# Optimization experiments

Measured on AMD Instinct MI355X. Metric: run time of the kernel, lower is better.

Reference implementation:

```python
import jax, jax.numpy as jnp
import numpy as np

RD = 3  # rec_depth


def _conv_block(x, w, b):
    # x: [B, T, C] -> Conv1d(same padding for odd kernel) + ReLU.
    # AdaptiveMaxPool1d(T) on a length-T input is the identity, so it is omitted.
    pad = (w.shape[-1] - 1) // 2
    xc = jnp.transpose(x, (0, 2, 1))  # [B, C, T]
    out = jax.lax.conv_general_dilated(xc, w, (1,), [(pad, pad)],
                                       dimension_numbers=('NCH', 'OIH', 'NCH'))
    out = jax.nn.relu(out + b[None, :, None])
    return jnp.transpose(out, (0, 2, 1))  # [B, T, n_filters]


def _rhn_cell(x_in, s, WH, WT, RHw, RHb, RTw, RTb):
    # Coupled-gate RHN cell: RD micro-steps of gated highway updates.
    preds = []
    for l in range(RD):
        if l == 0:
            h = jnp.tanh(x_in @ WH + s @ RHw[l] + RHb[l])
            t = jax.nn.sigmoid(x_in @ WT + s @ RTw[l] + RTb[l])
        else:
            h = jnp.tanh(s @ RHw[l] + RHb[l])
            t = jax.nn.sigmoid(s @ RTw[l] + RTb[l])
        s = h * t + (1.0 - t) * s
        preds.append(s)
    return s, preds


def _forward(x, y, conv0_w, conv0_b, conv1_w, conv1_b, c2e_w, c2e_b,
             enc_WH, enc_WT, enc_RHw, enc_RHb, enc_RTw, enc_RTb,
             dec_WH, dec_WT, dec_RHw, dec_RHb, dec_RTw, dec_RTb,
             Tk_w, Uk_w, Uk_b, vk_w, vk_b,
             Wt_w, Vt_w, Vt_b, W_w, W_b, V_w, V_b):
    x = _conv_block(x, conv0_w, conv0_b)
    x = _conv_block(x, conv1_w, conv1_b)
    x = x @ c2e_w + c2e_b                          # [B, T, enc_input_size]
    B, T, _ = x.shape
    NE = enc_WH.shape[1]
    ND = dec_WH.shape[1]

    # ---- RHN encoder: scan over time, emit state after every rec-depth step ----
    def enc_step(s, x_t):
        s, preds = _rhn_cell(x_t, s, enc_WH, enc_WT, enc_RHw, enc_RHb, enc_RTw, enc_RTb)
        return s, jnp.stack(preds, axis=-1)        # [B, NE, RD]

    _, hw = jax.lax.scan(enc_step, jnp.zeros((B, NE), x.dtype), jnp.transpose(x, (1, 0, 2)))
    h = jnp.transpose(hw, (1, 0, 2, 3))            # [B, T, NE, RD] == h_T_L

    # Encoder-side attention projections are decoder-time-invariant: precompute.
    Uh = jnp.einsum('btnr,rnm->rbtm', h, Uk_w) + Uk_b[:, None, None, :]  # [RD, B, T, NE]

    # ---- attentive RHN decoder ----
    def dec_step(carry, y_t):
        s, _ = carry
        Ts = jnp.einsum('bd,rdm->rbm', s, Tk_w)    # T_k(s) broadcast over T
        e = jnp.einsum('rbtm,rm->rbt', jnp.tanh(Uh + Ts[:, :, None, :]), vk_w) \
            + vk_b[:, None, None]                  # [RD, B, T]
        alpha = jax.nn.softmax(e, axis=-1)         # softmax over T
        d = jnp.einsum('rbt,btnr->rbn', alpha, h)  # [RD, B, NE]
        d = jnp.transpose(d, (1, 0, 2)).reshape(B, -1)  # [B, RD*NE], k-major blocks
        y_til = y_t @ Wt_w + d @ Vt_w + Vt_b
        s, _ = _rhn_cell(y_til, s, dec_WH, dec_WT, dec_RHw, dec_RHb, dec_RTw, dec_RTb)
        return (s, d), None

    init = (jnp.zeros((B, ND), x.dtype), jnp.zeros((B, RD * NE), x.dtype))
    (s, d), _ = jax.lax.scan(dec_step, init, jnp.transpose(y, (1, 0, 2)))
    return s @ W_w + W_b + d @ V_w + V_b           # [B, target_feats]


def setup_inputs() -> dict:
    ks = jax.random.split(jax.random.key(0), 24)
    B, T, F, TF = 256, 256, 16, 1
    NF, EI, NE, ND, FS = 64, 64, 128, 128, 5

    def rn(i, shape, s=0.1):
        return jax.random.normal(ks[i], shape, jnp.float32) * s

    z = lambda *shape: jnp.zeros(shape, jnp.float32)
    return {
        'x': jax.random.normal(ks[0], (B, T, F), jnp.float32),
        'y': jax.random.normal(ks[1], (B, T, TF), jnp.float32),
        'conv0_w': rn(2, (NF, F, FS)), 'conv0_b': z(NF),
        'conv1_w': rn(3, (NF, NF, FS)), 'conv1_b': z(NF),
        'c2e_w': rn(4, (NF, EI)), 'c2e_b': z(EI),
        'enc_WH': rn(5, (EI, NE)), 'enc_WT': rn(6, (EI, NE)),
        'enc_RHw': rn(7, (RD, NE, NE)), 'enc_RHb': z(RD, NE),
        'enc_RTw': rn(8, (RD, NE, NE)), 'enc_RTb': z(RD, NE),
        'dec_WH': rn(9, (TF, ND)), 'dec_WT': rn(10, (TF, ND)),
        'dec_RHw': rn(11, (RD, ND, ND)), 'dec_RHb': z(RD, ND),
        'dec_RTw': rn(12, (RD, ND, ND)), 'dec_RTb': z(RD, ND),
        'Tk_w': rn(13, (RD, ND, NE)),
        'Uk_w': rn(14, (RD, NE, NE)), 'Uk_b': z(RD, NE),
        'vk_w': rn(15, (RD, NE)), 'vk_b': z(RD),
        'Wt_w': rn(16, (TF, TF)),
        'Vt_w': rn(17, (RD * NE, TF)), 'Vt_b': z(TF),
        'W_w': rn(18, (ND, TF)), 'W_b': z(TF),
        'V_w': rn(19, (RD * NE, TF)), 'V_b': z(TF),
    }


def reference(x, y, conv0_w, conv0_b, conv1_w, conv1_b, c2e_w, c2e_b,
              enc_WH, enc_WT, enc_RHw, enc_RHb, enc_RTw, enc_RTb,
              dec_WH, dec_WT, dec_RHw, dec_RHb, dec_RTw, dec_RTb,
              Tk_w, Uk_w, Uk_b, vk_w, vk_b,
              Wt_w, Vt_w, Vt_b, W_w, W_b, V_w, V_b):
    return _forward(x, y, conv0_w, conv0_b, conv1_w, conv1_b, c2e_w, c2e_b,
                    enc_WH, enc_WT, enc_RHw, enc_RHb, enc_RTw, enc_RTb,
                    dec_WH, dec_WT, dec_RHw, dec_RHb, dec_RTw, dec_RTb,
                    Tk_w, Uk_w, Uk_b, vk_w, vk_b,
                    Wt_w, Vt_w, Vt_b, W_w, W_b, V_w, V_b)
```

## Files before the change

kernel.cpp:

```cpp
#include <hip/hip_runtime.h>
#include <cstdint>

#define DEV __device__ __forceinline__

typedef unsigned short ushort8 __attribute__((ext_vector_type(8)));
typedef unsigned int uint32;

#if __has_builtin(__builtin_amdgcn_rcpf)
DEV float rcp_fast(float x) { return __builtin_amdgcn_rcpf(x); }
#else
DEV float rcp_fast(float x) { return 1.f / x; }
#endif
#if __has_builtin(__builtin_amdgcn_exp2f)
DEV float exp2_fast(float x) { return __builtin_amdgcn_exp2f(x); }
#else
DEV float exp2_fast(float x) { return exp2f(x); }
#endif

#define SCALE2LOG2E 2.8853900817779268f
#define LOG2E 1.4426950408889634f

DEV float tanh_fast(float x) {
  float z = exp2_fast(x * SCALE2LOG2E);
  return 1.f - 2.f * rcp_fast(z + 1.f);
}
DEV float sigmoid_fast(float x) {
  return rcp_fast(1.f + exp2_fast(-LOG2E * x));
}

DEV unsigned short f2bf(float f) {
  uint32 u = __float_as_uint(f);
  u += 0x7FFFu + ((u >> 16) & 1u);
  return (unsigned short)(u >> 16);
}
DEV float bf2f(unsigned short s) { return __uint_as_float(((uint32)s) << 16); }
DEV float bf2f_lo(uint32 u) { return __uint_as_float(u << 16); }
DEV float bf2f_hi(uint32 u) { return __uint_as_float(u & 0xFFFF0000u); }

__global__ __launch_bounds__(256) void k_prep(const float* __restrict__ RHw,
                                              const float* __restrict__ RTw,
                                              uint32* __restrict__ out) {
  int i = blockIdx.x * 256 + threadIdx.x;
  if (i >= 49152) return;
  int g = i / 24576, rem = i % 24576;
  int l = rem / 8192, n2 = (rem >> 7) & 63, m = rem & 127;
  const float* W = g ? RTw : RHw;
  float w0 = W[(size_t)(l * 128 + 2 * n2) * 128 + m];
  float w1 = W[(size_t)(l * 128 + 2 * n2 + 1) * 128 + m];
  out[i] = (uint32)f2bf(w0) | ((uint32)f2bf(w1) << 16);
}

__global__ __launch_bounds__(256) void k_conv0(
    const float* __restrict__ x, const float* __restrict__ w,
    const float* __restrict__ bias, float* __restrict__ out) {
  __shared__ float wl[16 * 5 * 64];
  __shared__ float xl[68 * 16];
  const int blk = blockIdx.x;
  const int b = blk >> 2, tt = blk & 3;
  const int tid = threadIdx.x;
  for (int i = tid; i < 5120; i += 256) {
    int o = i / 80, rem = i % 80, ii = rem / 5, kk = rem % 5;
    wl[(ii * 5 + kk) * 64 + o] = w[i];
  }
  const int t0 = tt * 64;
  for (int i = tid; i < 68 * 16; i += 256) {
    int row = i >> 4, c = i & 15;
    int t = t0 - 2 + row;
    xl[i] = (t >= 0 && t < 256) ? x[((b << 8) + t) * 16 + c] : 0.f;
  }
  __syncthreads();
  const int o = tid & 63, tr = tid >> 6;
  for (int j = 0; j < 16; ++j) {
    int tl = tr * 16 + j;
    float acc = bias[o];
#pragma unroll
    for (int kk = 0; kk < 5; ++kk)
#pragma unroll
      for (int ii = 0; ii < 16; ++ii)
        acc += xl[(tl + kk) * 16 + ii] * wl[(ii * 5 + kk) * 64 + o];
    out[((b << 8) + t0 + tl) * 64 + o] = fmaxf(acc, 0.f);
  }
}

__global__ __launch_bounds__(256) void k_conv1(
    const float* __restrict__ in0, const float* __restrict__ w,
    const float* __restrict__ bias, float* __restrict__ out) {
  __shared__ float wl[64 * 5 * 64];
  __shared__ float xl[68 * 64];
  const int blk = blockIdx.x;
  const int b = blk >> 2, tt = blk & 3;
  const int tid = threadIdx.x;
  for (int i = tid; i < 64 * 5 * 64; i += 256) {
    int o = i / 320, rem = i % 320, ii = rem / 5, kk = rem % 5;
    wl[(ii * 5 + kk) * 64 + o] = w[i];
  }
  const int t0 = tt * 64;
  for (int i = tid; i < 68 * 64; i += 256) {
    int row = i >> 6, c = i & 63;
    int t = t0 - 2 + row;
    xl[i] = (t >= 0 && t < 256) ? in0[((b << 8) + t) * 64 + c] : 0.f;
  }
  __syncthreads();
  const int o = tid & 63, tr = tid >> 6;
  for (int j = 0; j < 16; ++j) {
    int tl = tr * 16 + j;
    float acc = bias[o];
    for (int kk = 0; kk < 5; ++kk) {
#pragma unroll 16
      for (int ii = 0; ii < 64; ++ii)
        acc += xl[(tl + kk) * 64 + ii] * wl[(ii * 5 + kk) * 64 + o];
    }
    out[((b << 8) + t0 + tl) * 64 + o] = fmaxf(acc, 0.f);
  }
}

__global__ __launch_bounds__(256) void k_c2e_proj(
    const float* __restrict__ in1, const float* __restrict__ cw,
    const float* __restrict__ cb, const float* __restrict__ WH,
    const float* __restrict__ WT, float* __restrict__ xph,
    float* __restrict__ xpt) {
  __shared__ float xin[64 * 64];
  __shared__ float w1[64 * 64];
  __shared__ float xe[64 * 64];
  __shared__ float wh[64 * 128];
  __shared__ float wt[64 * 128];
  const int blk = blockIdx.x;
  const int b = blk >> 2, tt = blk & 3;
  const int tid = threadIdx.x;
  for (int i = tid; i < 4096; i += 256) {
    xin[i] = in1[(size_t)(((b << 8) + tt * 64)) * 64 + i];
    w1[i] = cw[i];
  }
  for (int i = tid; i < 8192; i += 256) {
    wh[i] = WH[i];
    wt[i] = WT[i];
  }
  __syncthreads();
  {
    const int o = tid & 63, tr = tid >> 6;
    for (int j = 0; j < 16; ++j) {
      int tl = tr * 16 + j;
      float acc = cb[o];
#pragma unroll 16
      for (int k = 0; k < 64; ++k) acc += xin[tl * 64 + k] * w1[k * 64 + o];
      xe[tl * 64 + o] = acc;
    }
  }
  __syncthreads();
  {
    const int m = tid & 127, hf = tid >> 7;
    for (int j = 0; j < 32; ++j) {
      int tl = hf * 32 + j;
      float a0 = 0.f, a1 = 0.f;
#pragma unroll 16
      for (int k = 0; k < 64; ++k) {
        float xv = xe[tl * 64 + k];
        a0 += xv * wh[k * 128 + m];
        a1 += xv * wt[k * 128 + m];
      }
      size_t oidx = (size_t)((b << 8) + tt * 64 + tl) * 128 + m;
      xph[oidx] = a0;
      xpt[oidx] = a1;
    }
  }
}

__global__ __launch_bounds__(512, 2) void k_encoder(
    const float* __restrict__ xph, const float* __restrict__ xpt,
    const float* __restrict__ RHw, const float* __restrict__ RHb,
    const float* __restrict__ RTw, const float* __restrict__ RTb,
    unsigned short* __restrict__ h_bf) {
  const int b = blockIdx.x;
  const int tid = threadIdx.x;
  const int g = tid >> 8;
  const int m = (tid >> 1) & 127;
  const int hf = tid & 1;
  const float* W = g ? RTw : RHw;
  const float* Bb = g ? RTb : RHb;
  const float* XP = g ? xpt : xph;
  float wreg[3][64];
#pragma unroll
  for (int l = 0; l < 3; ++l)
#pragma unroll
    for (int j = 0; j < 64; ++j)
      wreg[l][j] = W[(size_t)(l * 128 + hf * 64 + j) * 128 + m];
  float bias[3];
#pragma unroll
  for (int l = 0; l < 3; ++l) bias[l] = Bb[l * 128 + m];

  __shared__ float s_lds[128];
  __shared__ float hg[128];
  __shared__ float tg[128];
  if (tid < 128) s_lds[tid] = 0.f;
  __syncthreads();

  for (int t = 0; t < 256; ++t) {
    const float xp = XP[(size_t)((b << 8) + t) * 128 + m];
#pragma unroll
    for (int l = 0; l < 3; ++l) {
      float acc = (hf == 0) ? (bias[l] + (l == 0 ? xp : 0.f)) : 0.f;
      const float* sp = s_lds + hf * 64;
#pragma unroll
      for (int j = 0; j < 64; ++j) acc += sp[j] * wreg[l][j];
      float tot = acc + __shfl_xor(acc, 1);
      if (hf == 0) {
        if (g == 0) hg[m] = tanh_fast(tot);
        else        tg[m] = sigmoid_fast(tot);
      }
      __syncthreads();
      if (tid < 128) {
        float tv = tg[tid];
        float sn = hg[tid] * tv + (1.f - tv) * s_lds[tid];
        s_lds[tid] = sn;
        h_bf[((size_t)(b * 3 + l) * 256 + t) * 128 + tid] = f2bf(sn);
      }
      __syncthreads();
    }
  }
}

__global__ __launch_bounds__(256, 2) void k_uh(
    const unsigned short* __restrict__ h_bf, const float* __restrict__ Uk_w,
    const float* __restrict__ Uk_b, unsigned short* __restrict__ Uh_bf) {
  __shared__ float wl[128 * 128];
  __shared__ float hl[32 * 128];
  const int blk = blockIdx.x;
  const int b = blk / 3, r = blk % 3;
  const int tid = threadIdx.x;
  for (int i = tid; i < 16384; i += 256) wl[i] = Uk_w[(size_t)r * 16384 + i];
  const int m = tid & 127, tr = tid >> 7;
  const float ub = Uk_b[r * 128 + m];
  for (int tt = 0; tt < 8; ++tt) {
    const size_t hbase = ((size_t)(b * 3 + r) * 256 + tt * 32) * 128;
    __syncthreads();
    const ushort8* hv = (const ushort8*)(h_bf + hbase);
    for (int i = tid; i < 512; i += 256) {
      ushort8 u = hv[i];
#pragma unroll
      for (int j = 0; j < 8; ++j) hl[i * 8 + j] = bf2f(u[j]);
    }
    __syncthreads();
    for (int j = 0; j < 16; ++j) {
      int tl = tr * 16 + j;
      float acc = ub;
#pragma unroll 16
      for (int n = 0; n < 128; ++n) acc += hl[tl * 128 + n] * wl[n * 128 + m];
      Uh_bf[hbase + (size_t)tl * 128 + m] = f2bf(acc * SCALE2LOG2E);
    }
  }
}

__global__ __launch_bounds__(768) void k_hv(
    const unsigned short* __restrict__ h_bf, const float* __restrict__ Vt_w,
    const float* __restrict__ V_w, float* __restrict__ hv,
    float* __restrict__ hv2) {
  __shared__ float vt[384], vw[384];
  const int b = blockIdx.x, tid = threadIdx.x;
  if (tid < 384) {
    vt[tid] = Vt_w[tid];
    vw[tid] = V_w[tid];
  }
  __syncthreads();
  const int r = tid >> 8;
  const uint2* hp = (const uint2*)(h_bf + ((size_t)b * 768 + tid) * 128);
  const float* vtp = vt + r * 128;
  const float* vwp = vw + r * 128;
  float a1 = 0.f, a2 = 0.f;
#pragma unroll 8
  for (int q = 0; q < 32; ++q) {
    uint2 u = hp[q];
    int m = q * 4;
    float h0 = bf2f_lo(u.x), h1 = bf2f_hi(u.x);
    float h2 = bf2f_lo(u.y), h3 = bf2f_hi(u.y);
    a1 += vtp[m] * h0 + vtp[m + 1] * h1 + vtp[m + 2] * h2 + vtp[m + 3] * h3;
    a2 += vwp[m] * h0 + vwp[m + 1] * h1 + vwp[m + 2] * h2 + vwp[m + 3] * h3;
  }
  hv[(size_t)b * 768 + tid] = a1;
  hv2[(size_t)b * 768 + tid] = a2;
}

__global__ __launch_bounds__(1024, 4) void k_decoder(
    const float* __restrict__ y, const unsigned short* __restrict__ Uh_bf,
    const float* __restrict__ hv_g, const float* __restrict__ hv2_g,
    const float* __restrict__ Tk_w, const float* __restrict__ vk_w,
    const float* __restrict__ vk_b, const float* __restrict__ Wt_w,
    const float* __restrict__ Vt_b, const float* __restrict__ WHd,
    const float* __restrict__ WTd, const uint32* __restrict__ cellw,
    const float* __restrict__ RHb, const float* __restrict__ RTb,
    const float* __restrict__ W_w, const float* __restrict__ W_b,
    const float* __restrict__ V_b, float* __restrict__ out) {
  const int b = blockIdx.x, tid = threadIdx.x;

  __shared__ uint32 tk_lds[24576];
  __shared__ __align__(8) float Ts_lds[3 * 136];
  __shared__ __align__(8) float vk_pad[3 * 136];
  __shared__ __align__(8) float a_lds[768];
  __shared__ float hv_lds[768], hv2_lds[768];
  __shared__ __align__(8) float s_lds[128];
  __shared__ float cpart[8 * 128];
  __shared__ float bias_lds[1024];
  __shared__ float y_lds[256];
  __shared__ float redN[12], redD[12], redN2[12];
  __shared__ float svk_lds[3];
  __shared__ float ytil_lds;

  for (int i = tid; i < 24576; i += 1024) {
    int r = i >> 13, rem = i & 8191, j = rem >> 7, m = rem & 127;
    float g0 = Tk_w[(size_t)r * 16384 + (2 * j) * 128 + m] * SCALE2LOG2E;
    float g1 = Tk_w[(size_t)r * 16384 + (2 * j + 1) * 128 + m] * SCALE2LOG2E;
    tk_lds[r * 8192 + m * 64 + (j ^ (m & 31))] =
        (uint32)f2bf(g0) | ((uint32)f2bf(g1) << 16);
  }
  if (tid < 384) {
    int r = tid >> 7, m = tid & 127;
    vk_pad[r * 136 + (m >> 5) * 34 + (m & 31)] = -2.f * vk_w[tid];
    bias_lds[tid] = RHb[tid];
    bias_lds[384 + tid] = RTb[tid];
  }
  if (tid < 3) {
    float sv = vk_b[tid];
    for (int m = 0; m < 128; ++m) sv += vk_w[tid * 128 + m];
    svk_lds[tid] = sv;
  }
  if (tid < 128) {
    bias_lds[768 + tid] = WHd[tid];
    bias_lds[896 + tid] = WTd[tid];
    s_lds[tid] = 0.f;
  }
  if (tid < 256) y_lds[tid] = y[(b << 8) + tid];
  if (tid < 768) {
    hv_lds[tid] = hv_g[(size_t)b * 768 + tid];
    hv2_lds[tid] = hv2_g[(size_t)b * 768 + tid];
  }
  const float wt0 = Wt_w[0], vtb0 = Vt_b[0];

  const int t_e4 = tid >> 2, q4 = tid & 3;
  uint32 ureg[3][16];
#pragma unroll
  for (int r = 0; r < 3; ++r) {
    const uint4* up = (const uint4*)(Uh_bf +
        ((size_t)(b * 3 + r) * 256 + t_e4) * 128 + q4 * 32);
#pragma unroll
    for (int q = 0; q < 4; ++q) {
      uint4 v = up[q];
      ureg[r][4 * q + 0] = v.x;
      ureg[r][4 * q + 1] = v.y;
      ureg[r][4 * q + 2] = v.z;
      ureg[r][4 * q + 3] = v.w;
    }
  }
  uint32 zr;
  asm volatile("s_mov_b32 %0, 0" : "=s"(zr));
#pragma unroll
  for (int r = 0; r < 3; ++r)
#pragma unroll
    for (int q = 0; q < 16; ++q) ureg[r][q] ^= zr;
  __syncthreads();

  const int lane = tid & 63, wv = tid >> 6;
  const int r3t = (tid >> 8) & 3, m2 = (tid >> 1) & 127, p2 = tid & 1;
  const int gc = tid >> 9, ch = (tid >> 7) & 3, mc = tid & 127;
  const uint32* Wc = cellw + gc * 24576 + mc;
  const int n2base = ch * 16;

  for (int step = 0; step < 256; ++step) {
    if (tid < 768) {
      const uint32* tkp = tk_lds + r3t * 8192 + m2 * 64;
      const int swz = m2 & 31;
      const float* sp = s_lds + p2 * 64;
      const int jb = p2 * 32;
      float acc = 0.f;
#pragma unroll 8
      for (int jj = 0; jj < 32; ++jj) {
        uint32 w = tkp[(jb + jj) ^ swz];
        float2 sv = *(const float2*)(sp + 2 * jj);
        acc += sv.x * bf2f_lo(w) + sv.y * bf2f_hi(w);
      }
      float tot = acc + __shfl_xor(acc, 1);
      if (p2 == 0) Ts_lds[r3t * 136 + (m2 >> 5) * 34 + (m2 & 31)] = tot;
    }
    __syncthreads();
    {
      float er[3];
#pragma unroll
      for (int r = 0; r < 3; ++r) {
        const float2* ts2 = (const float2*)(Ts_lds + r * 136 + q4 * 34);
        const float2* vk2 = (const float2*)(vk_pad + r * 136 + q4 * 34);
        float acc0 = 0.f, acc1 = 0.f;
#pragma unroll
        for (int j = 0; j < 16; ++j) {
          uint32 w = ureg[r][j];
          float2 t2 = ts2[j], v2 = vk2[j];
          float z0 = exp2_fast(bf2f_lo(w) + t2.x);
          float z1 = exp2_fast(bf2f_hi(w) + t2.y);
          acc0 += v2.x * rcp_fast(z0 + 1.f);
          acc1 += v2.y * rcp_fast(z1 + 1.f);
        }
        float a = acc0 + acc1;
        a += __shfl_xor(a, 1);
        a += __shfl_xor(a, 2);
        er[r] = a;
      }
      if (q4 == 0) {
#pragma unroll
        for (int r = 0; r < 3; ++r) a_lds[r * 256 + t_e4] = er[r] + svk_lds[r];
      }
    }
    __syncthreads();
    {
      float pn = 0.f, pd = 0.f, pn2 = 0.f;
      if (tid < 768) {
        float p = __expf(a_lds[tid]);
        pd = p;
        pn = p * hv_lds[tid];
        if (step == 255) pn2 = p * hv2_lds[tid];
      }
#pragma unroll
      for (int off = 32; off; off >>= 1) {
        pn += __shfl_xor(pn, off);
        pd += __shfl_xor(pd, off);
      }
      if (step == 255) {
#pragma unroll
        for (int off = 32; off; off >>= 1) pn2 += __shfl_xor(pn2, off);
        if (lane == 0 && wv < 12) redN2[wv] = pn2;
      }
      if (lane == 0 && wv < 12) {
        redN[wv] = pn;
        redD[wv] = pd;
      }
    }
    __syncthreads();
    const float2* sp2 = (const float2*)s_lds;
#pragma unroll
    for (int l = 0; l < 3; ++l) {
      {
        float acc = 0.f;
        const uint32* wp = Wc + (size_t)(l * 64 + n2base) * 128;
#pragma unroll 8
        for (int n2 = 0; n2 < 16; ++n2) {
          uint32 w = wp[(size_t)n2 * 128];
          float2 sv = sp2[n2base + n2];
          acc += sv.x * bf2f_lo(w) + sv.y * bf2f_hi(w);
        }
        cpart[(gc * 4 + ch) * 128 + mc] = acc;
        if (l == 0 && tid == 0) {
          float yt = y_lds[step] * wt0 + vtb0;
#pragma unroll
          for (int r = 0; r < 3; ++r) {
            float ns = redN[4 * r] + redN[4 * r + 1] + redN[4 * r + 2] + redN[4 * r + 3];
            float ds = redD[4 * r] + redD[4 * r + 1] + redD[4 * r + 2] + redD[4 * r + 3];
            yt += ns * rcp_fast(ds);
          }
          ytil_lds = yt;
        }
      }
      __syncthreads();
      if (tid < 128) {
        float ha = cpart[tid] + cpart[128 + tid] + cpart[256 + tid] +
                   cpart[384 + tid] + bias_lds[l * 128 + tid];
        float ta = cpart[512 + tid] + cpart[640 + tid] + cpart[768 + tid] +
                   cpart[896 + tid] + bias_lds[384 + l * 128 + tid];
        if (l == 0) {
          float yt = ytil_lds;
          ha += yt * bias_lds[768 + tid];
          ta += yt * bias_lds[896 + tid];
        }
        float hvv = tanh_fast(ha);
        float tv = sigmoid_fast(ta);
        s_lds[tid] = hvv * tv + (1.f - tv) * s_lds[tid];
      }
      __syncthreads();
    }
  }
  if (tid < 64) {
    float acc = s_lds[tid] * W_w[tid] + s_lds[tid + 64] * W_w[tid + 64];
#pragma unroll
    for (int off = 32; off; off >>= 1) acc += __shfl_xor(acc, off);
    if (tid == 0) {
      float o = acc + W_b[0] + V_b[0];
#pragma unroll
      for (int r = 0; r < 3; ++r) {
        float ns = redN2[4 * r] + redN2[4 * r + 1] + redN2[4 * r + 2] + redN2[4 * r + 3];
        float ds = redD[4 * r] + redD[4 * r + 1] + redD[4 * r + 2] + redD[4 * r + 3];
        o += ns * rcp_fast(ds);
      }
      out[b] = o;
    }
  }
}

extern "C" void kernel_launch(void* const* d_in, const int* in_sizes, int n_in,
                              void* d_out, int out_size, void* d_ws,
                              size_t ws_size, hipStream_t stream) {
  (void)in_sizes; (void)n_in; (void)out_size; (void)ws_size;
  const float* x    = (const float*)d_in[0];
  const float* y    = (const float*)d_in[1];
  const float* c0w  = (const float*)d_in[2];
  const float* c0b  = (const float*)d_in[3];
  const float* c1w  = (const float*)d_in[4];
  const float* c1b  = (const float*)d_in[5];
  const float* c2ew = (const float*)d_in[6];
  const float* c2eb = (const float*)d_in[7];
  const float* eWH  = (const float*)d_in[8];
  const float* eWT  = (const float*)d_in[9];
  const float* eRHw = (const float*)d_in[10];
  const float* eRHb = (const float*)d_in[11];
  const float* eRTw = (const float*)d_in[12];
  const float* eRTb = (const float*)d_in[13];
  const float* dWH  = (const float*)d_in[14];
  const float* dWT  = (const float*)d_in[15];
  const float* dRHw = (const float*)d_in[16];
  const float* dRHb = (const float*)d_in[17];
  const float* dRTw = (const float*)d_in[18];
  const float* dRTb = (const float*)d_in[19];
  const float* Tk   = (const float*)d_in[20];
  const float* Ukw  = (const float*)d_in[21];
  const float* Ukb  = (const float*)d_in[22];
  const float* vkw  = (const float*)d_in[23];
  const float* vkb  = (const float*)d_in[24];
  const float* Wtw  = (const float*)d_in[25];
  const float* Vtw  = (const float*)d_in[26];
  const float* Vtb  = (const float*)d_in[27];
  const float* Ww   = (const float*)d_in[28];
  const float* Wb   = (const float*)d_in[29];
  const float* Vw   = (const float*)d_in[30];
  const float* Vb   = (const float*)d_in[31];
  float* out = (float*)d_out;
  float* ws = (float*)d_ws;

  unsigned short* h_bf  = (unsigned short*)ws;
  unsigned short* Uh_bf = (unsigned short*)(ws + 12582912);
  float* xph = ws + 12582912;
  float* xpt = ws + 20971520;
  float* c0o = ws + 29360128;
  float* hv  = ws + 29360128;
  float* hv2 = ws + 30146560;
  float* c1o = ws + 33554432;
  uint32* cellw = (uint32*)(ws + 37748736);

  k_prep<<<192, 256, 0, stream>>>(dRHw, dRTw, cellw);
  k_conv0<<<1024, 256, 0, stream>>>(x, c0w, c0b, c0o);
  k_conv1<<<1024, 256, 0, stream>>>(c0o, c1w, c1b, c1o);
  k_c2e_proj<<<1024, 256, 0, stream>>>(c1o, c2ew, c2eb, eWH, eWT, xph, xpt);
  k_encoder<<<256, 512, 0, stream>>>(xph, xpt, eRHw, eRHb, eRTw, eRTb, h_bf);
  k_uh<<<768, 256, 0, stream>>>(h_bf, Ukw, Ukb, Uh_bf);
  k_hv<<<256, 768, 0, stream>>>(h_bf, Vtw, Vw, hv, hv2);
  k_decoder<<<256, 1024, 0, stream>>>(y, Uh_bf, hv, hv2, Tk, vkw, vkb, Wtw,
                                      Vtb, dWH, dWT, cellw, dRHb, dRTb,
                                      Ww, Wb, Vb, out);
}
```

Before: 4.901 ms.

## Restructure decoder cell matvec with shuffle reductions and double-buffered state

The decoder RHN cell matvec now gives each group of 8 threads one output row, with each thread reading contiguous uint4 weight vectors under a new k_prep layout. Partial sums are combined with warp shuffles instead of an LDS partial buffer plus a second phase. This removes one __syncthreads per micro-step, and a double-buffered state vector makes that safe. Ts and vk are interleaved into float4 entries so the attention-score loop issues fewer, wider LDS loads. Every thread also computes ytil redundantly instead of one thread writing it to shared memory.

```diff
diff --git a/kernel.cpp b/kernel.cpp
--- a/kernel.cpp
+++ b/kernel.cpp
@@ -43,7 +43,8 @@
   int i = blockIdx.x * 256 + threadIdx.x;
   if (i >= 49152) return;
   int g = i / 24576, rem = i % 24576;
-  int l = rem / 8192, n2 = (rem >> 7) & 63, m = rem & 127;
+  int l = rem / 8192, rem2 = rem & 8191;
+  int m = rem2 >> 6, n2 = rem2 & 63;
   const float* W = g ? RTw : RHw;
   float w0 = W[(size_t)(l * 128 + 2 * n2) * 128 + m];
   float w1 = W[(size_t)(l * 128 + 2 * n2 + 1) * 128 + m];
@@ -292,17 +293,14 @@
   const int b = blockIdx.x, tid = threadIdx.x;
 
   __shared__ uint32 tk_lds[24576];
-  __shared__ __align__(8) float Ts_lds[3 * 136];
-  __shared__ __align__(8) float vk_pad[3 * 136];
+  __shared__ __align__(16) float4 tsvk4[3 * 4 * 17];
+  __shared__ __align__(16) float s_buf[2][128];
   __shared__ __align__(8) float a_lds[768];
   __shared__ float hv_lds[768], hv2_lds[768];
-  __shared__ __align__(8) float s_lds[128];
-  __shared__ float cpart[8 * 128];
   __shared__ float bias_lds[1024];
   __shared__ float y_lds[256];
   __shared__ float redN[12], redD[12], redN2[12];
   __shared__ float svk_lds[3];
-  __shared__ float ytil_lds;
 
   for (int i = tid; i < 24576; i += 1024) {
     int r = i >> 13, rem = i & 8191, j = rem >> 7, m = rem & 127;
@@ -311,21 +309,26 @@
     tk_lds[r * 8192 + m * 64 + (j ^ (m & 31))] =
         (uint32)f2bf(g0) | ((uint32)f2bf(g1) << 16);
   }
-  if (tid < 384) {
-    int r = tid >> 7, m = tid & 127;
-    vk_pad[r * 136 + (m >> 5) * 34 + (m & 31)] = -2.f * vk_w[tid];
-    bias_lds[tid] = RHb[tid];
-    bias_lds[384 + tid] = RTb[tid];
+  if (tid < 192) {
+    int r = tid >> 6, rem = tid & 63, q4i = rem >> 4, j = rem & 15;
+    int mb = q4i * 32 + 2 * j;
+    tsvk4[(r * 4 + q4i) * 17 + j].z = -2.f * vk_w[r * 128 + mb];
+    tsvk4[(r * 4 + q4i) * 17 + j].w = -2.f * vk_w[r * 128 + mb + 1];
   }
   if (tid < 3) {
     float sv = vk_b[tid];
     for (int m = 0; m < 128; ++m) sv += vk_w[tid * 128 + m];
     svk_lds[tid] = sv;
   }
+  if (tid < 384) {
+    bias_lds[tid] = RHb[tid];
+    bias_lds[384 + tid] = RTb[tid];
+  }
   if (tid < 128) {
     bias_lds[768 + tid] = WHd[tid];
     bias_lds[896 + tid] = WTd[tid];
-    s_lds[tid] = 0.f;
+    s_buf[0][tid] = 0.f;
+    s_buf[1][tid] = 0.f;
   }
   if (tid < 256) y_lds[tid] = y[(b << 8) + tid];
   if (tid < 768) {
@@ -359,42 +362,45 @@
 
   const int lane = tid & 63, wv = tid >> 6;
   const int r3t = (tid >> 8) & 3, m2 = (tid >> 1) & 127, p2 = tid & 1;
-  const int gc = tid >> 9, ch = (tid >> 7) & 3, mc = tid & 127;
-  const uint32* Wc = cellw + gc * 24576 + mc;
-  const int n2base = ch * 16;
+  const int mC = tid >> 3, sub = tid & 7, gC = sub >> 2, chC = sub & 3;
+  const uint32* wb0 = cellw + ((size_t)(gC * 3) << 13) + (mC << 6) + (chC << 4);
+  float* scur = s_buf[0];
+  float* snxt = s_buf[1];
 
   for (int step = 0; step < 256; ++step) {
     if (tid < 768) {
       const uint32* tkp = tk_lds + r3t * 8192 + m2 * 64;
       const int swz = m2 & 31;
-      const float* sp = s_lds + p2 * 64;
+      const float4* sp4 = (const float4*)scur + p2 * 16;
       const int jb = p2 * 32;
       float acc = 0.f;
 #pragma unroll 8
-      for (int jj = 0; jj < 32; ++jj) {
-        uint32 w = tkp[(jb + jj) ^ swz];
-        float2 sv = *(const float2*)(sp + 2 * jj);
-        acc += sv.x * bf2f_lo(w) + sv.y * bf2f_hi(w);
+      for (int k = 0; k < 16; ++k) {
+        float4 f4 = sp4[k];
+        uint32 w0 = tkp[(jb + 2 * k) ^ swz];
+        uint32 w1 = tkp[(jb + 2 * k + 1) ^ swz];
+        acc += f4.x * bf2f_lo(w0) + f4.y * bf2f_hi(w0) +
+               f4.z * bf2f_lo(w1) + f4.w * bf2f_hi(w1);
       }
       float tot = acc + __shfl_xor(acc, 1);
-      if (p2 == 0) Ts_lds[r3t * 136 + (m2 >> 5) * 34 + (m2 & 31)] = tot;
+      if (p2 == 0)
+        ((float*)&tsvk4[(r3t * 4 + (m2 >> 5)) * 17 + ((m2 >> 1) & 15)])[m2 & 1] = tot;
     }
     __syncthreads();
     {
       float er[3];
 #pragma unroll
       for (int r = 0; r < 3; ++r) {
-        const float2* ts2 = (const float2*)(Ts_lds + r * 136 + q4 * 34);
-        const float2* vk2 = (const float2*)(vk_pad + r * 136 + q4 * 34);
+        const float4* tv4 = tsvk4 + (r * 4 + q4) * 17;
         float acc0 = 0.f, acc1 = 0.f;
 #pragma unroll
         for (int j = 0; j < 16; ++j) {
           uint32 w = ureg[r][j];
-          float2 t2 = ts2[j], v2 = vk2[j];
-          float z0 = exp2_fast(bf2f_lo(w) + t2.x);
-          float z1 = exp2_fast(bf2f_hi(w) + t2.y);
-          acc0 += v2.x * rcp_fast(z0 + 1.f);
-          acc1 += v2.y * rcp_fast(z1 + 1.f);
+          float4 q = tv4[j];
+          float z0 = exp2_fast(bf2f_lo(w) + q.x);
+          float z1 = exp2_fast(bf2f_hi(w) + q.y);
+          acc0 += q.z * rcp_fast(z0 + 1.f);
+          acc1 += q.w * rcp_fast(z1 + 1.f);
         }
         float a = acc0 + acc1;
         a += __shfl_xor(a, 1);
@@ -431,50 +437,48 @@
       }
     }
     __syncthreads();
-    const float2* sp2 = (const float2*)s_lds;
+    float ytil = y_lds[step] * wt0 + vtb0;
+#pragma unroll
+    for (int r = 0; r < 3; ++r) {
+      float ns = redN[4 * r] + redN[4 * r + 1] + redN[4 * r + 2] + redN[4 * r + 3];
+      float ds = redD[4 * r] + redD[4 * r + 1] + redD[4 * r + 2] + redD[4 * r + 3];
+      ytil += ns * rcp_fast(ds);
+    }
 #pragma unroll
     for (int l = 0; l < 3; ++l) {
-      {
-        float acc = 0.f;
-        const uint32* wp = Wc + (size_t)(l * 64 + n2base) * 128;
-#pragma unroll 8
-        for (int n2 = 0; n2 < 16; ++n2) {
-          uint32 w = wp[(size_t)n2 * 128];
-          float2 sv = sp2[n2base + n2];
-          acc += sv.x * bf2f_lo(w) + sv.y * bf2f_hi(w);
-        }
-        cpart[(gc * 4 + ch) * 128 + mc] = acc;
-        if (l == 0 && tid == 0) {
-          float yt = y_lds[step] * wt0 + vtb0;
-#pragma unroll
-          for (int r = 0; r < 3; ++r) {
-            float ns = redN[4 * r] + redN[4 * r + 1] + redN[4 * r + 2] + redN[4 * r + 3];
-            float ds = redD[4 * r] + redD[4 * r + 1] + redD[4 * r + 2] + redD[4 * r + 3];
-            yt += ns * rcp_fast(ds);
-          }
-          ytil_lds = yt;
-        }
-      }
+      const uint4* wp = (const uint4*)(wb0 + (l << 13));
+      const float4* sp4 = (const float4*)scur + chC * 8;
+      float acc = 0.f;
+#pragma unroll
+      for (int q = 0; q < 4; ++q) {
+        uint4 w4 = wp[q];
+        float4 fa = sp4[2 * q], fb = sp4[2 * q + 1];
+        acc += fa.x * bf2f_lo(w4.x) + fa.y * bf2f_hi(w4.x) +
+               fa.z * bf2f_lo(w4.y) + fa.w * bf2f_hi(w4.y) +
+               fb.x * bf2f_lo(w4.z) + fb.y * bf2f_hi(w4.z) +
+               fb.z * bf2f_lo(w4.w) + fb.w * bf2f_hi(w4.w);
+      }
+      acc += __shfl_xor(acc, 1);
+      acc += __shfl_xor(acc, 2);
+      float other = __shfl_xor(acc, 4);
+      float hsum = gC ? other : acc;
+      float tsum = gC ? acc : other;
+      float s_old = scur[mC];
+      float ha = hsum + bias_lds[l * 128 + mC];
+      float ta = tsum + bias_lds[384 + l * 128 + mC];
+      if (l == 0) {
+        ha += ytil * bias_lds[768 + mC];
+        ta += ytil * bias_lds[896 + mC];
+      }
+      float hvv = tanh_fast(ha);
+      float tv = sigmoid_fast(ta);
+      if (sub == 0) snxt[mC] = hvv * tv + (1.f - tv) * s_old;
       __syncthreads();
-      if (tid < 128) {
-        float ha = cpart[tid] + cpart[128 + tid] + cpart[256 + tid] +
-                   cpart[384 + tid] + bias_lds[l * 128 + tid];
-        float ta = cpart[512 + tid] + cpart[640 + tid] + cpart[768 + tid] +
-                   cpart[896 + tid] + bias_lds[384 + l * 128 + tid];
-        if (l == 0) {
-          float yt = ytil_lds;
-          ha += yt * bias_lds[768 + tid];
-          ta += yt * bias_lds[896 + tid];
-        }
-        float hvv = tanh_fast(ha);
-        float tv = sigmoid_fast(ta);
-        s_lds[tid] = hvv * tv + (1.f - tv) * s_lds[tid];
-      }
-      __syncthreads();
+      float* tmp = scur; scur = snxt; snxt = tmp;
     }
   }
   if (tid < 64) {
-    float acc = s_lds[tid] * W_w[tid] + s_lds[tid + 64] * W_w[tid + 64];
+    float acc = scur[tid] * W_w[tid] + scur[tid + 64] * W_w[tid + 64];
 #pragma unroll
     for (int off = 32; off; off >>= 1) acc += __shfl_xor(acc, off);
     if (tid == 0) {
```

New measurement: 8.192 ms. 1.67x slower.

## Reduce RHN decoder cell partials with wave shuffles and double-buffer state

Applied to the files above, without the earlier changes.

The decoder's recurrent cell matvec is remapped so the 8 partial sums for each output (4 chunks × H/T gates) sit in adjacent lanes and are reduced with shuffles, not written to a shared partial array and summed by 128 threads. The state vector is double-buffered, so each micro-step needs one barrier instead of two, and every thread computes the attention scalar redundantly instead of one thread broadcasting it. This removes one block-wide sync per micro-step, the cpart LDS traffic and the serialized 128-thread tail. In exchange, all threads run the tanh/sigmoid and the ytil reduction redundantly, and the weight loads become strided across lanes (mC = tid>>3), which may hurt global-load coalescing.

```diff
diff --git a/kernel.cpp b/kernel.cpp
--- a/kernel.cpp
+++ b/kernel.cpp
@@ -296,13 +296,11 @@
   __shared__ __align__(8) float vk_pad[3 * 136];
   __shared__ __align__(8) float a_lds[768];
   __shared__ float hv_lds[768], hv2_lds[768];
-  __shared__ __align__(8) float s_lds[128];
-  __shared__ float cpart[8 * 128];
+  __shared__ __align__(8) float s_buf[2][128];
   __shared__ float bias_lds[1024];
   __shared__ float y_lds[256];
   __shared__ float redN[12], redD[12], redN2[12];
   __shared__ float svk_lds[3];
-  __shared__ float ytil_lds;
 
   for (int i = tid; i < 24576; i += 1024) {
     int r = i >> 13, rem = i & 8191, j = rem >> 7, m = rem & 127;
@@ -325,7 +323,8 @@
   if (tid < 128) {
     bias_lds[768 + tid] = WHd[tid];
     bias_lds[896 + tid] = WTd[tid];
-    s_lds[tid] = 0.f;
+    s_buf[0][tid] = 0.f;
+    s_buf[1][tid] = 0.f;
   }
   if (tid < 256) y_lds[tid] = y[(b << 8) + tid];
   if (tid < 768) {
@@ -359,15 +358,15 @@
 
   const int lane = tid & 63, wv = tid >> 6;
   const int r3t = (tid >> 8) & 3, m2 = (tid >> 1) & 127, p2 = tid & 1;
-  const int gc = tid >> 9, ch = (tid >> 7) & 3, mc = tid & 127;
-  const uint32* Wc = cellw + gc * 24576 + mc;
-  const int n2base = ch * 16;
+  const int mC = tid >> 3, sub = tid & 7, gC = (sub >> 2) & 1, chC = sub & 3;
+  const uint32* Wc = cellw + gC * 24576 + mC;
+  int spb = 0;
 
   for (int step = 0; step < 256; ++step) {
     if (tid < 768) {
       const uint32* tkp = tk_lds + r3t * 8192 + m2 * 64;
       const int swz = m2 & 31;
-      const float* sp = s_lds + p2 * 64;
+      const float* sp = s_buf[spb] + p2 * 64;
       const int jb = p2 * 32;
       float acc = 0.f;
 #pragma unroll 8
@@ -431,50 +430,50 @@
       }
     }
     __syncthreads();
-    const float2* sp2 = (const float2*)s_lds;
 #pragma unroll
     for (int l = 0; l < 3; ++l) {
-      {
-        float acc = 0.f;
-        const uint32* wp = Wc + (size_t)(l * 64 + n2base) * 128;
+      const float* sc = s_buf[spb];
+      const float2* sp2 = (const float2*)sc;
+      float ytil = 0.f;
+      if (l == 0) {
+        ytil = y_lds[step] * wt0 + vtb0;
+#pragma unroll
+        for (int r = 0; r < 3; ++r) {
+          float ns = redN[4 * r] + redN[4 * r + 1] + redN[4 * r + 2] + redN[4 * r + 3];
+          float ds = redD[4 * r] + redD[4 * r + 1] + redD[4 * r + 2] + redD[4 * r + 3];
+          ytil += ns * rcp_fast(ds);
+        }
+      }
+      float acc = 0.f;
+      const uint32* wp = Wc + (size_t)(l * 64 + chC * 16) * 128;
 #pragma unroll 8
-        for (int n2 = 0; n2 < 16; ++n2) {
-          uint32 w = wp[(size_t)n2 * 128];
-          float2 sv = sp2[n2base + n2];
-          acc += sv.x * bf2f_lo(w) + sv.y * bf2f_hi(w);
-        }
-        cpart[(gc * 4 + ch) * 128 + mc] = acc;
-        if (l == 0 && tid == 0) {
-          float yt = y_lds[step] * wt0 + vtb0;
-#pragma unroll
-          for (int r = 0; r < 3; ++r) {
-            float ns = redN[4 * r] + redN[4 * r + 1] + redN[4 * r + 2] + redN[4 * r + 3];
-            float ds = redD[4 * r] + redD[4 * r + 1] + redD[4 * r + 2] + redD[4 * r + 3];
-            yt += ns * rcp_fast(ds);
-          }
-          ytil_lds = yt;
-        }
-      }
+      for (int n2 = 0; n2 < 16; ++n2) {
+        uint32 w = wp[(size_t)n2 * 128];
+        float2 sv = sp2[chC * 16 + n2];
+        acc += sv.x * bf2f_lo(w) + sv.y * bf2f_hi(w);
+      }
+      acc += __shfl_xor(acc, 1);
+      acc += __shfl_xor(acc, 2);
+      float other = __shfl_xor(acc, 4);
+      float hsum = gC ? other : acc;
+      float tsum = gC ? acc : other;
+      float s_old = sc[mC];
+      float ha = hsum + bias_lds[l * 128 + mC];
+      float ta = tsum + bias_lds[384 + l * 128 + mC];
+      if (l == 0) {
+        ha += ytil * bias_lds[768 + mC];
+        ta += ytil * bias_lds[896 + mC];
+      }
+      float hvv = tanh_fast(ha);
+      float tv = sigmoid_fast(ta);
+      if (sub == 0) s_buf[spb ^ 1][mC] = hvv * tv + (1.f - tv) * s_old;
       __syncthreads();
-      if (tid < 128) {
-        float ha = cpart[tid] + cpart[128 + tid] + cpart[256 + tid] +
-                   cpart[384 + tid] + bias_lds[l * 128 + tid];
-        float ta = cpart[512 + tid] + cpart[640 + tid] + cpart[768 + tid] +
-                   cpart[896 + tid] + bias_lds[384 + l * 128 + tid];
-        if (l == 0) {
-          float yt = ytil_lds;
-          ha += yt * bias_lds[768 + tid];
-          ta += yt * bias_lds[896 + tid];
-        }
-        float hvv = tanh_fast(ha);
-        float tv = sigmoid_fast(ta);
-        s_lds[tid] = hvv * tv + (1.f - tv) * s_lds[tid];
-      }
-      __syncthreads();
+      spb ^= 1;
     }
   }
   if (tid < 64) {
-    float acc = s_lds[tid] * W_w[tid] + s_lds[tid + 64] * W_w[tid + 64];
+    const float* sc = s_buf[spb];
+    float acc = sc[tid] * W_w[tid] + sc[tid + 64] * W_w[tid + 64];
 #pragma unroll
     for (int off = 32; off; off >>= 1) acc += __shfl_xor(acc, off);
     if (tid == 0) {
```

Result: slower. 8.689 ms (+77.3%).
